# Performance work log

Measured on AMD Instinct MI355X. Metric: run time of the kernel, lower is better.

Reference implementation:

```python
import jax, jax.numpy as jnp
import numpy as np

B, S, H = 2, 2048, 2048
NH, NKV, HD = 16, 4, 128
SCALING = HD ** -0.5


def rotate_half(x):
    x1, x2 = jnp.split(x, 2, axis=-1)
    return jnp.concatenate((-x2, x1), axis=-1)


def apply_rope(t, cos, sin):
    # t: [B, nh, S, HD]; cos/sin: [B, S, HD] -> unsqueeze head dim
    c = cos[:, None, :, :]
    s = sin[:, None, :, :]
    return t * c + rotate_half(t) * s


def setup_inputs() -> dict:
    key = jax.random.key(0)
    k1, k2, k3, k4, k5 = jax.random.split(key, 5)
    hidden_states = jax.random.normal(k1, (B, S, H), dtype=jnp.float32)
    # real RoPE tables
    inv_freq = 1.0 / (10000.0 ** (jnp.arange(0, HD, 2, dtype=jnp.float32) / HD))
    pos = jnp.arange(S, dtype=jnp.float32)
    freqs = jnp.einsum('s,d->sd', pos, inv_freq)              # [S, HD/2]
    emb = jnp.concatenate((freqs, freqs), axis=-1)            # [S, HD]
    cos = jnp.broadcast_to(jnp.cos(emb)[None], (B, S, HD))
    sin = jnp.broadcast_to(jnp.sin(emb)[None], (B, S, HD))
    # additive causal mask [B, 1, S, S]
    causal = jnp.triu(jnp.full((S, S), -1e9, dtype=jnp.float32), k=1)
    attention_mask = jnp.broadcast_to(causal[None, None], (B, 1, S, S))
    sc = 0.02
    wq = jax.random.normal(k2, (NH * HD, H), dtype=jnp.float32) * sc
    wk = jax.random.normal(k3, (NKV * HD, H), dtype=jnp.float32) * sc
    wv = jax.random.normal(k4, (NKV * HD, H), dtype=jnp.float32) * sc
    wo = jax.random.normal(k5, (H, NH * HD), dtype=jnp.float32) * sc
    return {"hidden_states": hidden_states, "cos": cos, "sin": sin,
            "attention_mask": attention_mask, "wq": wq, "wk": wk, "wv": wv, "wo": wo}


def reference(hidden_states, cos, sin, attention_mask, wq, wk, wv, wo):
    x = hidden_states
    # fused-style QKV projections (nn.Linear: x @ W.T), split heads -> [B, nh, S, HD]
    q = (x @ wq.T).reshape(B, S, NH, HD).transpose(0, 2, 1, 3)
    k = (x @ wk.T).reshape(B, S, NKV, HD).transpose(0, 2, 1, 3)
    v = (x @ wv.T).reshape(B, S, NKV, HD).transpose(0, 2, 1, 3)
    q = apply_rope(q, cos, sin)
    k = apply_rope(k, cos, sin)
    # GQA: repeat KV heads (repeat_kv)
    n_rep = NH // NKV
    k = jnp.repeat(k, n_rep, axis=1)
    v = jnp.repeat(v, n_rep, axis=1)
    scores = jnp.einsum('bhqd,bhkd->bhqk', q, k) * SCALING + attention_mask
    attn = jax.nn.softmax(scores.astype(jnp.float32), axis=-1).astype(q.dtype)
    out = jnp.einsum('bhqk,bhkd->bhqd', attn, v)
    out = out.transpose(0, 2, 1, 3).reshape(B, S, NH * HD)
    out = out @ wo.T
    return (out, attn)
```

## Files before the change

### kernel.cpp

```cpp
#include <hip/hip_runtime.h>
#include <cstdint>
#include <cstddef>

typedef __bf16 bf16;
typedef __attribute__((ext_vector_type(8))) __bf16 bf16x8;
typedef __attribute__((ext_vector_type(4))) __bf16 bf16x4;
typedef __attribute__((ext_vector_type(4))) float f32x4;

constexpr int B_ = 2, S_ = 2048, H_ = 2048, NH_ = 16, NKV_ = 4, HD_ = 128;
constexpr float SCALE_ = 0.08838834764831845f;

#define GLDS16(g, l)                                                        \
  __builtin_amdgcn_global_load_lds(                                         \
      (const __attribute__((address_space(1))) void*)(g),                   \
      (__attribute__((address_space(3))) void*)(l), 16, 0, 0)

__global__ void cvt_kernel(const float* __restrict__ src, bf16* __restrict__ dst, int n4) {
  int stride = gridDim.x * blockDim.x;
  for (int i = blockIdx.x * blockDim.x + threadIdx.x; i < n4; i += stride) {
    float4 v = reinterpret_cast<const float4*>(src)[i];
    bf16x4 o;
    o[0] = (bf16)v.x; o[1] = (bf16)v.y; o[2] = (bf16)v.z; o[3] = (bf16)v.w;
    reinterpret_cast<bf16x4*>(dst)[i] = o;
  }
}

template <int EPI>
__global__ __launch_bounds__(256) void gemm_bt(const bf16* __restrict__ A,
                                               const bf16* __restrict__ Bm, int K,
                                               bf16* __restrict__ qb, bf16* __restrict__ kb,
                                               bf16* __restrict__ vtb, float* __restrict__ Cout) {
  __shared__ __align__(16) bf16 As[128 * 64];
  __shared__ __align__(16) bf16 Bs[128 * 64];
  const int tid = threadIdx.x;
  const int lane = tid & 63;
  const int wid = tid >> 6;
  const int m0 = blockIdx.x * 128;
  const int n0 = blockIdx.y * 128;
  const int wm = (wid >> 1) * 64, wn = (wid & 1) * 64;
  const int r = lane & 15, g = lane >> 4;
  f32x4 acc[4][4] = {};

  for (int kt = 0; kt < K; kt += 64) {
    __syncthreads();
#pragma unroll
    for (int i = 0; i < 4; ++i) {
      int cb = wid * 256 + i * 64;
      int c = cb + lane;
      int row = c >> 3, cs = (c & 7) ^ (row & 7);
      const bf16* ga = A + (size_t)(m0 + row) * K + kt + cs * 8;
      GLDS16(ga, As + cb * 8);
      const bf16* gb = Bm + (size_t)(n0 + row) * K + kt + cs * 8;
      GLDS16(gb, Bs + cb * 8);
    }
    asm volatile("s_waitcnt vmcnt(0)" ::: "memory");
    __syncthreads();
#pragma unroll
    for (int ks = 0; ks < 2; ++ks) {
      bf16x8 af[4], bfr[4];
#pragma unroll
      for (int fm = 0; fm < 4; ++fm)
        af[fm] = *(const bf16x8*)(As + (wm + fm * 16 + r) * 64 + (((ks * 4 + g) ^ (r & 7)) << 3));
#pragma unroll
      for (int fn = 0; fn < 4; ++fn)
        bfr[fn] = *(const bf16x8*)(Bs + (wn + fn * 16 + r) * 64 + (((ks * 4 + g) ^ (r & 7)) << 3));
#pragma unroll
      for (int fm = 0; fm < 4; ++fm)
#pragma unroll
        for (int fn = 0; fn < 4; ++fn)
          acc[fm][fn] = __builtin_amdgcn_mfma_f32_16x16x32_bf16(af[fm], bfr[fn], acc[fm][fn], 0, 0, 0);
    }
  }

#pragma unroll
  for (int fm = 0; fm < 4; ++fm)
#pragma unroll
    for (int fn = 0; fn < 4; ++fn)
#pragma unroll
      for (int rr = 0; rr < 4; ++rr) {
        int mm = m0 + wm + fm * 16 + g * 4 + rr;
        int nn = n0 + wn + fn * 16 + r;
        float v = acc[fm][fn][rr];
        if (EPI == 1) {
          Cout[(size_t)mm * 2048 + nn] = v;
        } else {
          int b = mm >> 11, s = mm & (S_ - 1);
          int d = nn & 127;
          if (nn < 2048) {
            int h = nn >> 7;
            qb[(((size_t)b * NH_ + h) * S_ + s) * HD_ + d] = (bf16)v;
          } else if (nn < 2560) {
            int h = (nn - 2048) >> 7;
            kb[(((size_t)b * NKV_ + h) * S_ + s) * HD_ + d] = (bf16)v;
          } else {
            int h = (nn - 2560) >> 7;
            vtb[(((size_t)b * NKV_ + h) * HD_ + d) * S_ + s] = (bf16)v;
          }
        }
      }
}

__global__ void rope_kernel(bf16* __restrict__ qb, bf16* __restrict__ kb,
                            const float* __restrict__ cosp, const float* __restrict__ sinp) {
  const int NQ = B_ * NH_ * S_;
  const int NK = B_ * NKV_ * S_;
  int tot = (NQ + NK) * 64;
  for (int t = blockIdx.x * blockDim.x + threadIdx.x; t < tot; t += gridDim.x * blockDim.x) {
    int d = t & 63;
    int rid = t >> 6;
    bf16* base;
    int b, s;
    if (rid < NQ) {
      base = qb + (size_t)rid * HD_;
      s = rid & (S_ - 1);
      b = rid >> 15;
    } else {
      int r2 = rid - NQ;
      base = kb + (size_t)r2 * HD_;
      s = r2 & (S_ - 1);
      b = r2 >> 13;
    }
    float c = cosp[((size_t)b * S_ + s) * HD_ + d];
    float sn = sinp[((size_t)b * S_ + s) * HD_ + d];
    float x1 = (float)base[d], x2 = (float)base[d + 64];
    base[d] = (bf16)(x1 * c - x2 * sn);
    base[d + 64] = (bf16)(x2 * c + x1 * sn);
  }
}

__global__ __launch_bounds__(256) void attn_kernel(const bf16* __restrict__ qb,
                                                   const bf16* __restrict__ kb,
                                                   const bf16* __restrict__ vtb,
                                                   bf16* __restrict__ aob,
                                                   float* __restrict__ attn_out) {
  __shared__ __align__(16) bf16 Qs[64 * 128];
  __shared__ __align__(16) bf16 Ks[64 * 128];
  __shared__ __align__(16) bf16 Vs[128 * 64];
  __shared__ __align__(16) bf16 Ps[64 * 64];
  const int bid = (blockIdx.x & 7) * 128 + (blockIdx.x >> 3);
  const int qt = 31 - (bid & 31);
  const int h = (bid >> 5) & 15;
  const int b = bid >> 9;
  const int kh = h >> 2;
  const int q0 = qt * 64;
  const int tid = threadIdx.x, lane = tid & 63, wid = tid >> 6;
  const int r = lane & 15, g = lane >> 4;

  const bf16* qsrc = qb + (((size_t)b * NH_ + h) * S_ + q0) * HD_;
  const bf16* kbase = kb + ((size_t)b * NKV_ + kh) * S_ * HD_;
  const bf16* vbase = vtb + ((size_t)b * NKV_ + kh) * (size_t)HD_ * S_;

#pragma unroll
  for (int i = 0; i < 4; ++i) {
    int cb = wid * 256 + i * 64, c = cb + lane;
    int row = c >> 4, cs = (c & 15) ^ (row & 7);
    GLDS16(qsrc + row * 128 + cs * 8, Qs + cb * 8);
  }

  float mrow[4], lrow[4];
#pragma unroll
  for (int i = 0; i < 4; ++i) { mrow[i] = -3e38f; lrow[i] = 0.f; }

  for (int kt = 0; kt <= qt; ++kt) {
    const int k0 = kt * 64;
    __syncthreads();
#pragma unroll
    for (int i = 0; i < 4; ++i) {
      int cb = wid * 256 + i * 64, c = cb + lane;
      int row = c >> 4, cs = (c & 15) ^ (row & 7);
      GLDS16(kbase + (size_t)k0 * HD_ + row * 128 + cs * 8, Ks + cb * 8);
    }
    asm volatile("s_waitcnt vmcnt(0)" ::: "memory");
    __syncthreads();
    f32x4 sacc[4] = {};
#pragma unroll
    for (int ks = 0; ks < 4; ++ks) {
      bf16x8 a = *(const bf16x8*)(Qs + (wid * 16 + r) * 128 + (((ks * 4 + g) ^ (r & 7)) << 3));
#pragma unroll
      for (int fn = 0; fn < 4; ++fn) {
        bf16x8 bb = *(const bf16x8*)(Ks + (fn * 16 + r) * 128 + (((ks * 4 + g) ^ (r & 7)) << 3));
        sacc[fn] = __builtin_amdgcn_mfma_f32_16x16x32_bf16(a, bb, sacc[fn], 0, 0, 0);
      }
    }
    float sv[4][4], tmax[4];
#pragma unroll
    for (int rr = 0; rr < 4; ++rr) tmax[rr] = -3e38f;
#pragma unroll
    for (int fn = 0; fn < 4; ++fn)
#pragma unroll
      for (int rr = 0; rr < 4; ++rr) {
        float s = sacc[fn][rr] * SCALE_;
        if (kt == qt && (fn * 16 + r) > (wid * 16 + g * 4 + rr)) s = -3e38f;
        sv[fn][rr] = s;
        tmax[rr] = fmaxf(tmax[rr], s);
      }
#pragma unroll
    for (int m = 1; m <= 8; m <<= 1)
#pragma unroll
      for (int rr = 0; rr < 4; ++rr) tmax[rr] = fmaxf(tmax[rr], __shfl_xor(tmax[rr], m));
#pragma unroll
    for (int rr = 0; rr < 4; ++rr) {
      float mn = fmaxf(mrow[rr], tmax[rr]);
      float sum = 0.f;
#pragma unroll
      for (int fn = 0; fn < 4; ++fn) sum += __expf(sv[fn][rr] - mn);
#pragma unroll
      for (int m = 1; m <= 8; m <<= 1) sum += __shfl_xor(sum, m);
      lrow[rr] = lrow[rr] * __expf(mrow[rr] - mn) + sum;
      mrow[rr] = mn;
    }
  }

  float rl[4];
#pragma unroll
  for (int rr = 0; rr < 4; ++rr) rl[rr] = 1.0f / lrow[rr];

  f32x4 oacc[8] = {};
  const size_t arow0 = ((size_t)(b * NH_ + h) * S_ + q0) * S_;
  const int trow = tid >> 2;
  const int tcb = (tid & 3) * 16;
  for (int kt = 0; kt <= qt; ++kt) {
    const int k0 = kt * 64;
    __syncthreads();
#pragma unroll
    for (int i = 0; i < 4; ++i) {
      int cb = wid * 256 + i * 64, c = cb + lane;
      int krow = c >> 4, kcs = (c & 15) ^ (krow & 7);
      GLDS16(kbase + (size_t)k0 * HD_ + krow * 128 + kcs * 8, Ks + cb * 8);
      int vrow = c >> 3, vcs = (c & 7) ^ (vrow & 7);
      GLDS16(vbase + (size_t)vrow * S_ + k0 + vcs * 8, Vs + cb * 8);
    }
    asm volatile("s_waitcnt vmcnt(0)" ::: "memory");
    __syncthreads();
    f32x4 sacc[4] = {};
#pragma unroll
    for (int ks = 0; ks < 4; ++ks) {
      bf16x8 a = *(const bf16x8*)(Qs + (wid * 16 + r) * 128 + (((ks * 4 + g) ^ (r & 7)) << 3));
#pragma unroll
      for (int fn = 0; fn < 4; ++fn) {
        bf16x8 bb = *(const bf16x8*)(Ks + (fn * 16 + r) * 128 + (((ks * 4 + g) ^ (r & 7)) << 3));
        sacc[fn] = __builtin_amdgcn_mfma_f32_16x16x32_bf16(a, bb, sacc[fn], 0, 0, 0);
      }
    }
#pragma unroll
    for (int fn = 0; fn < 4; ++fn)
#pragma unroll
      for (int rr = 0; rr < 4; ++rr) {
        float s = sacc[fn][rr] * SCALE_;
        if (kt == qt && (fn * 16 + r) > (wid * 16 + g * 4 + rr)) s = -3e38f;
        float p = __expf(s - mrow[rr]) * rl[rr];
        int qrow = wid * 16 + g * 4 + rr;
        int col = fn * 16 + r;
        Ps[qrow * 64 + ((((col >> 3) ^ (qrow & 7)) << 3) | (col & 7))] = (bf16)p;
      }
    __syncthreads();
    {
      float* dst = attn_out + arow0 + (size_t)trow * S_ + k0 + tcb;
      int ch0 = tcb >> 3;
      bf16x8 p0 = *(const bf16x8*)(Ps + trow * 64 + ((ch0 ^ (trow & 7)) << 3));
      bf16x8 p1 = *(const bf16x8*)(Ps + trow * 64 + (((ch0 + 1) ^ (trow & 7)) << 3));
      float4 o0 = {(float)p0[0], (float)p0[1], (float)p0[2], (float)p0[3]};
      float4 o1 = {(float)p0[4], (float)p0[5], (float)p0[6], (float)p0[7]};
      float4 o2 = {(float)p1[0], (float)p1[1], (float)p1[2], (float)p1[3]};
      float4 o3 = {(float)p1[4], (float)p1[5], (float)p1[6], (float)p1[7]};
      *(float4*)(dst) = o0;
      *(float4*)(dst + 4) = o1;
      *(float4*)(dst + 8) = o2;
      *(float4*)(dst + 12) = o3;
    }
#pragma unroll
    for (int ks = 0; ks < 2; ++ks) {
      bf16x8 pa = *(const bf16x8*)(Ps + (wid * 16 + r) * 64 + (((ks * 4 + g) ^ (r & 7)) << 3));
#pragma unroll
      for (int fn = 0; fn < 8; ++fn) {
        bf16x8 vv = *(const bf16x8*)(Vs + (fn * 16 + r) * 64 + (((ks * 4 + g) ^ (r & 7)) << 3));
        oacc[fn] = __builtin_amdgcn_mfma_f32_16x16x32_bf16(pa, vv, oacc[fn], 0, 0, 0);
      }
    }
  }

  for (int kt = qt + 1; kt < 32; ++kt) {
#pragma unroll
    for (int i = 0; i < 4; ++i) {
      int c = i * 256 + tid;
      int row = c >> 4, col = c & 15;
      float4 z = {0.f, 0.f, 0.f, 0.f};
      *(float4*)(attn_out + arow0 + (size_t)row * S_ + kt * 64 + col * 4) = z;
    }
  }

#pragma unroll
  for (int fn = 0; fn < 8; ++fn)
#pragma unroll
    for (int rr = 0; rr < 4; ++rr) {
      int q = q0 + wid * 16 + g * 4 + rr;
      aob[((size_t)b * S_ + q) * 2048 + h * HD_ + fn * 16 + r] = (bf16)oacc[fn][rr];
    }
}

extern "C" void kernel_launch(void* const* d_in, const int* in_sizes, int n_in,
                              void* d_out, int out_size, void* d_ws, size_t ws_size,
                              hipStream_t stream) {
  const float* hidden = (const float*)d_in[0];
  const float* cosp = (const float*)d_in[1];
  const float* sinp = (const float*)d_in[2];
  const float* wq = (const float*)d_in[4];
  const float* wk = (const float*)d_in[5];
  const float* wv = (const float*)d_in[6];
  const float* wo = (const float*)d_in[7];
  float* out = (float*)d_out;
  float* attn = out + (size_t)B_ * S_ * H_;

  char* ws = (char*)d_ws;
  bf16* xb  = (bf16*)(ws);
  bf16* w3b = (bf16*)(ws + (16ull << 20));
  bf16* wob = (bf16*)(ws + (28ull << 20));
  bf16* qb  = (bf16*)(ws + (36ull << 20));
  bf16* kb  = (bf16*)(ws + (52ull << 20));
  bf16* vtb = (bf16*)(ws + (56ull << 20));
  bf16* aob = (bf16*)(ws + (60ull << 20));

  cvt_kernel<<<2048, 256, 0, stream>>>(hidden, xb, (B_ * S_ * H_) / 4);
  cvt_kernel<<<1024, 256, 0, stream>>>(wq, w3b, (2048 * 2048) / 4);
  cvt_kernel<<<512, 256, 0, stream>>>(wk, w3b + 2048 * 2048, (512 * 2048) / 4);
  cvt_kernel<<<512, 256, 0, stream>>>(wv, w3b + 2560 * 2048, (512 * 2048) / 4);
  cvt_kernel<<<1024, 256, 0, stream>>>(wo, wob, (2048 * 2048) / 4);

  gemm_bt<0><<<dim3(32, 24), 256, 0, stream>>>(xb, w3b, 2048, qb, kb, vtb, nullptr);
  rope_kernel<<<2048, 256, 0, stream>>>(qb, kb, cosp, sinp);
  attn_kernel<<<1024, 256, 0, stream>>>(qb, kb, vtb, aob, attn);
  gemm_bt<1><<<dim3(32, 16), 256, 0, stream>>>(aob, wob, 2048, nullptr, nullptr, nullptr, out);
}
```

Before: 401.6 us.

## Double-buffer GEMM and attention tiles, pair causal q-tiles, fuse conversion kernels

Merges the five fp32-to-bf16 conversion launches into one kernel. Double-buffers the GEMM LDS tiles so the next K-slice is fetched while the current one is multiplied, and adds a grouped block swizzle for L2 reuse. The attention kernel now keeps Q in registers, double-buffers K/V tiles, raises wave priority around MFMA sections, and has each block handle a short and a long causal q-tile pair (p and 31-p) to balance work across 512 blocks. It trades higher LDS use and more complex wait/barrier logic for overlap of loads with compute.

```diff
diff --git a/kernel.cpp b/kernel.cpp
--- a/kernel.cpp
+++ b/kernel.cpp
@@ -15,61 +15,83 @@
       (const __attribute__((address_space(1))) void*)(g),                   \
       (__attribute__((address_space(3))) void*)(l), 16, 0, 0)
 
-__global__ void cvt_kernel(const float* __restrict__ src, bf16* __restrict__ dst, int n4) {
-  int stride = gridDim.x * blockDim.x;
-  for (int i = blockIdx.x * blockDim.x + threadIdx.x; i < n4; i += stride) {
-    float4 v = reinterpret_cast<const float4*>(src)[i];
+#define VMCNT0 asm volatile("s_waitcnt vmcnt(0)" ::: "memory")
+#define VMCNT4 asm volatile("s_waitcnt vmcnt(4)" ::: "memory")
+#define LGKM0 asm volatile("s_waitcnt lgkmcnt(0)" ::: "memory")
+#define BAR __builtin_amdgcn_s_barrier()
+
+__global__ void cvt_all(const float* __restrict__ hs, const float* __restrict__ wq,
+                        const float* __restrict__ wk, const float* __restrict__ wv,
+                        const float* __restrict__ wo, bf16* __restrict__ xb,
+                        bf16* __restrict__ w3b, bf16* __restrict__ wob) {
+  const int stride = gridDim.x * blockDim.x;
+  for (int i = blockIdx.x * blockDim.x + threadIdx.x; i < 4718592; i += stride) {
+    const float4* s; bf16x4* d; int j;
+    if (i < 2097152)      { s = (const float4*)hs; d = (bf16x4*)xb;            j = i; }
+    else if (i < 3145728) { s = (const float4*)wq; d = (bf16x4*)w3b;           j = i - 2097152; }
+    else if (i < 3407872) { s = (const float4*)wk; d = (bf16x4*)w3b + 1048576; j = i - 3145728; }
+    else if (i < 3670016) { s = (const float4*)wv; d = (bf16x4*)w3b + 1310720; j = i - 3407872; }
+    else                  { s = (const float4*)wo; d = (bf16x4*)wob;           j = i - 3670016; }
+    float4 v = s[j];
     bf16x4 o;
     o[0] = (bf16)v.x; o[1] = (bf16)v.y; o[2] = (bf16)v.z; o[3] = (bf16)v.w;
-    reinterpret_cast<bf16x4*>(dst)[i] = o;
+    d[j] = o;
   }
 }
 
 template <int EPI>
-__global__ __launch_bounds__(256) void gemm_bt(const bf16* __restrict__ A,
-                                               const bf16* __restrict__ Bm, int K,
-                                               bf16* __restrict__ qb, bf16* __restrict__ kb,
-                                               bf16* __restrict__ vtb, float* __restrict__ Cout) {
-  __shared__ __align__(16) bf16 As[128 * 64];
-  __shared__ __align__(16) bf16 Bs[128 * 64];
+__global__ __launch_bounds__(256, 2) void gemm_bt(const bf16* __restrict__ A,
+                                                  const bf16* __restrict__ Bm, int K,
+                                                  bf16* __restrict__ qb, bf16* __restrict__ kb,
+                                                  bf16* __restrict__ vtb, float* __restrict__ Cout) {
+  __shared__ __align__(16) bf16 As[2][128 * 64];
+  __shared__ __align__(16) bf16 Bs[2][128 * 64];
   const int tid = threadIdx.x;
   const int lane = tid & 63;
   const int wid = tid >> 6;
-  const int m0 = blockIdx.x * 128;
-  const int n0 = blockIdx.y * 128;
+  const int fid = blockIdx.y * 32 + blockIdx.x;
+  const int nwg = gridDim.y * 32;
+  const int swz = (fid & 7) * (nwg >> 3) + (fid >> 3);
+  const int m0 = (swz & 31) * 128;
+  const int n0 = (swz >> 5) * 128;
   const int wm = (wid >> 1) * 64, wn = (wid & 1) * 64;
   const int r = lane & 15, g = lane >> 4;
   f32x4 acc[4][4] = {};
 
-  for (int kt = 0; kt < K; kt += 64) {
-    __syncthreads();
+  auto STAGE = [&](int kt, int cc) {
 #pragma unroll
     for (int i = 0; i < 4; ++i) {
       int cb = wid * 256 + i * 64;
-      int c = cb + lane;
-      int row = c >> 3, cs = (c & 7) ^ (row & 7);
-      const bf16* ga = A + (size_t)(m0 + row) * K + kt + cs * 8;
-      GLDS16(ga, As + cb * 8);
-      const bf16* gb = Bm + (size_t)(n0 + row) * K + kt + cs * 8;
-      GLDS16(gb, Bs + cb * 8);
-    }
-    asm volatile("s_waitcnt vmcnt(0)" ::: "memory");
-    __syncthreads();
+      int c64 = cb + lane;
+      int row = c64 >> 3, cs = (c64 & 7) ^ (row & 7);
+      GLDS16(A + (size_t)(m0 + row) * K + kt + cs * 8, &As[cc][cb * 8]);
+      GLDS16(Bm + (size_t)(n0 + row) * K + kt + cs * 8, &Bs[cc][cb * 8]);
+    }
+  };
+
+  STAGE(0, 0);
+  VMCNT0; BAR;
+  int c = 0;
+#pragma unroll 1
+  for (int kt = 0; kt < K; kt += 64) {
+    if (kt + 64 < K) STAGE(kt + 64, c ^ 1);
 #pragma unroll
     for (int ks = 0; ks < 2; ++ks) {
       bf16x8 af[4], bfr[4];
 #pragma unroll
       for (int fm = 0; fm < 4; ++fm)
-        af[fm] = *(const bf16x8*)(As + (wm + fm * 16 + r) * 64 + (((ks * 4 + g) ^ (r & 7)) << 3));
+        af[fm] = *(const bf16x8*)(&As[c][(wm + fm * 16 + r) * 64 + (((ks * 4 + g) ^ (r & 7)) << 3)]);
 #pragma unroll
       for (int fn = 0; fn < 4; ++fn)
-        bfr[fn] = *(const bf16x8*)(Bs + (wn + fn * 16 + r) * 64 + (((ks * 4 + g) ^ (r & 7)) << 3));
+        bfr[fn] = *(const bf16x8*)(&Bs[c][(wn + fn * 16 + r) * 64 + (((ks * 4 + g) ^ (r & 7)) << 3)]);
 #pragma unroll
       for (int fm = 0; fm < 4; ++fm)
 #pragma unroll
         for (int fn = 0; fn < 4; ++fn)
           acc[fm][fn] = __builtin_amdgcn_mfma_f32_16x16x32_bf16(af[fm], bfr[fn], acc[fm][fn], 0, 0, 0);
     }
+    VMCNT0; BAR;
+    c ^= 1;
   }
 
 #pragma unroll
@@ -87,14 +109,14 @@
           int b = mm >> 11, s = mm & (S_ - 1);
           int d = nn & 127;
           if (nn < 2048) {
-            int h = nn >> 7;
-            qb[(((size_t)b * NH_ + h) * S_ + s) * HD_ + d] = (bf16)v;
+            int hh = nn >> 7;
+            qb[(((size_t)b * NH_ + hh) * S_ + s) * HD_ + d] = (bf16)v;
           } else if (nn < 2560) {
-            int h = (nn - 2048) >> 7;
-            kb[(((size_t)b * NKV_ + h) * S_ + s) * HD_ + d] = (bf16)v;
+            int hh = (nn - 2048) >> 7;
+            kb[(((size_t)b * NKV_ + hh) * S_ + s) * HD_ + d] = (bf16)v;
           } else {
-            int h = (nn - 2560) >> 7;
-            vtb[(((size_t)b * NKV_ + h) * HD_ + d) * S_ + s] = (bf16)v;
+            int hh = (nn - 2560) >> 7;
+            vtb[(((size_t)b * NKV_ + hh) * HD_ + d) * S_ + s] = (bf16)v;
           }
         }
       }
@@ -128,174 +150,216 @@
   }
 }
 
-__global__ __launch_bounds__(256) void attn_kernel(const bf16* __restrict__ qb,
-                                                   const bf16* __restrict__ kb,
-                                                   const bf16* __restrict__ vtb,
-                                                   bf16* __restrict__ aob,
-                                                   float* __restrict__ attn_out) {
-  __shared__ __align__(16) bf16 Qs[64 * 128];
-  __shared__ __align__(16) bf16 Ks[64 * 128];
-  __shared__ __align__(16) bf16 Vs[128 * 64];
+__global__ __launch_bounds__(256, 2) void attn_kernel(const bf16* __restrict__ qb,
+                                                      const bf16* __restrict__ kb,
+                                                      const bf16* __restrict__ vtb,
+                                                      bf16* __restrict__ aob,
+                                                      float* __restrict__ attn_out) {
+  __shared__ __align__(16) bf16 Ks[2][64 * 128];
+  __shared__ __align__(16) bf16 Vs[2][128 * 64];
   __shared__ __align__(16) bf16 Ps[64 * 64];
-  const int bid = (blockIdx.x & 7) * 128 + (blockIdx.x >> 3);
-  const int qt = 31 - (bid & 31);
-  const int h = (bid >> 5) & 15;
-  const int b = bid >> 9;
+  const int bid = (blockIdx.x & 7) * 64 + (blockIdx.x >> 3);
+  const int p = bid & 15;
+  const int h = (bid >> 4) & 15;
+  const int b = bid >> 8;
   const int kh = h >> 2;
-  const int q0 = qt * 64;
   const int tid = threadIdx.x, lane = tid & 63, wid = tid >> 6;
   const int r = lane & 15, g = lane >> 4;
 
-  const bf16* qsrc = qb + (((size_t)b * NH_ + h) * S_ + q0) * HD_;
   const bf16* kbase = kb + ((size_t)b * NKV_ + kh) * S_ * HD_;
   const bf16* vbase = vtb + ((size_t)b * NKV_ + kh) * (size_t)HD_ * S_;
 
-#pragma unroll
-  for (int i = 0; i < 4; ++i) {
-    int cb = wid * 256 + i * 64, c = cb + lane;
-    int row = c >> 4, cs = (c & 15) ^ (row & 7);
-    GLDS16(qsrc + row * 128 + cs * 8, Qs + cb * 8);
-  }
-
-  float mrow[4], lrow[4];
-#pragma unroll
-  for (int i = 0; i < 4; ++i) { mrow[i] = -3e38f; lrow[i] = 0.f; }
-
-  for (int kt = 0; kt <= qt; ++kt) {
-    const int k0 = kt * 64;
-    __syncthreads();
+  auto stageK = [&](int kt, int cc) {
 #pragma unroll
     for (int i = 0; i < 4; ++i) {
-      int cb = wid * 256 + i * 64, c = cb + lane;
-      int row = c >> 4, cs = (c & 15) ^ (row & 7);
-      GLDS16(kbase + (size_t)k0 * HD_ + row * 128 + cs * 8, Ks + cb * 8);
-    }
-    asm volatile("s_waitcnt vmcnt(0)" ::: "memory");
-    __syncthreads();
-    f32x4 sacc[4] = {};
-#pragma unroll
-    for (int ks = 0; ks < 4; ++ks) {
-      bf16x8 a = *(const bf16x8*)(Qs + (wid * 16 + r) * 128 + (((ks * 4 + g) ^ (r & 7)) << 3));
-#pragma unroll
-      for (int fn = 0; fn < 4; ++fn) {
-        bf16x8 bb = *(const bf16x8*)(Ks + (fn * 16 + r) * 128 + (((ks * 4 + g) ^ (r & 7)) << 3));
-        sacc[fn] = __builtin_amdgcn_mfma_f32_16x16x32_bf16(a, bb, sacc[fn], 0, 0, 0);
-      }
-    }
-    float sv[4][4], tmax[4];
-#pragma unroll
-    for (int rr = 0; rr < 4; ++rr) tmax[rr] = -3e38f;
-#pragma unroll
-    for (int fn = 0; fn < 4; ++fn)
+      int base = i * 256 + wid * 64;
+      int idx = base + lane;
+      int row = idx >> 4, ch = (idx & 15) ^ (row & 7);
+      GLDS16(kbase + (size_t)(kt * 64 + row) * HD_ + ch * 8, &Ks[cc][base * 8]);
+    }
+  };
+  auto stageV = [&](int kt, int cc) {
+#pragma unroll
+    for (int i = 0; i < 4; ++i) {
+      int base = i * 256 + wid * 64;
+      int idx = base + lane;
+      int row = idx >> 3, ch = (idx & 7) ^ (row & 7);
+      GLDS16(vbase + (size_t)row * S_ + kt * 64 + ch * 8, &Vs[cc][base * 8]);
+    }
+  };
+
+#pragma unroll 1
+  for (int sbi = 0; sbi < 2; ++sbi) {
+    const int qt = sbi ? 31 - p : p;
+    const int q0 = qt * 64;
+    const int nt = qt + 1;
+    const bf16* qsrc = qb + (((size_t)b * NH_ + h) * S_ + q0) * HD_;
+
+    bf16x8 qreg[4];
+#pragma unroll
+    for (int ks = 0; ks < 4; ++ks)
+      qreg[ks] = *(const bf16x8*)(qsrc + (wid * 16 + r) * HD_ + ks * 32 + g * 8);
+
+    float mrow[4], lrow[4];
+#pragma unroll
+    for (int rr = 0; rr < 4; ++rr) { mrow[rr] = -3e38f; lrow[rr] = 0.f; }
+
+    stageK(0, 0);
+    VMCNT0; BAR;
+    int c = 0;
+#pragma unroll 1
+    for (int kt = 0; kt < nt; ++kt) {
+      if (kt + 1 < nt) stageK(kt + 1, c ^ 1);
+      f32x4 sacc[4] = {};
+      __builtin_amdgcn_s_setprio(1);
+#pragma unroll
+      for (int ks = 0; ks < 4; ++ks)
+#pragma unroll
+        for (int fn = 0; fn < 4; ++fn) {
+          bf16x8 bb = *(const bf16x8*)(&Ks[c][(fn * 16 + r) * 128 + (((ks * 4 + g) ^ (r & 7)) << 3)]);
+          sacc[fn] = __builtin_amdgcn_mfma_f32_16x16x32_bf16(qreg[ks], bb, sacc[fn], 0, 0, 0);
+        }
+      __builtin_amdgcn_s_setprio(0);
+      const int k0 = kt * 64;
+      if (kt == nt - 1) {
+#pragma unroll
+        for (int fn = 0; fn < 4; ++fn)
+#pragma unroll
+          for (int rr = 0; rr < 4; ++rr) {
+            bool msk = (k0 + fn * 16 + r) > (q0 + wid * 16 + g * 4 + rr);
+            sacc[fn][rr] = msk ? -3e38f : sacc[fn][rr] * SCALE_;
+          }
+      } else {
+#pragma unroll
+        for (int fn = 0; fn < 4; ++fn)
+#pragma unroll
+          for (int rr = 0; rr < 4; ++rr) sacc[fn][rr] *= SCALE_;
+      }
+      float tmax[4] = {-3e38f, -3e38f, -3e38f, -3e38f};
+#pragma unroll
+      for (int fn = 0; fn < 4; ++fn)
+#pragma unroll
+        for (int rr = 0; rr < 4; ++rr) tmax[rr] = fmaxf(tmax[rr], sacc[fn][rr]);
+#pragma unroll
+      for (int m = 1; m <= 8; m <<= 1)
+#pragma unroll
+        for (int rr = 0; rr < 4; ++rr) tmax[rr] = fmaxf(tmax[rr], __shfl_xor(tmax[rr], m));
 #pragma unroll
       for (int rr = 0; rr < 4; ++rr) {
-        float s = sacc[fn][rr] * SCALE_;
-        if (kt == qt && (fn * 16 + r) > (wid * 16 + g * 4 + rr)) s = -3e38f;
-        sv[fn][rr] = s;
-        tmax[rr] = fmaxf(tmax[rr], s);
-      }
-#pragma unroll
-    for (int m = 1; m <= 8; m <<= 1)
-#pragma unroll
-      for (int rr = 0; rr < 4; ++rr) tmax[rr] = fmaxf(tmax[rr], __shfl_xor(tmax[rr], m));
-#pragma unroll
-    for (int rr = 0; rr < 4; ++rr) {
-      float mn = fmaxf(mrow[rr], tmax[rr]);
-      float sum = 0.f;
-#pragma unroll
-      for (int fn = 0; fn < 4; ++fn) sum += __expf(sv[fn][rr] - mn);
-#pragma unroll
-      for (int m = 1; m <= 8; m <<= 1) sum += __shfl_xor(sum, m);
-      lrow[rr] = lrow[rr] * __expf(mrow[rr] - mn) + sum;
-      mrow[rr] = mn;
-    }
-  }
-
-  float rl[4];
-#pragma unroll
-  for (int rr = 0; rr < 4; ++rr) rl[rr] = 1.0f / lrow[rr];
-
-  f32x4 oacc[8] = {};
-  const size_t arow0 = ((size_t)(b * NH_ + h) * S_ + q0) * S_;
-  const int trow = tid >> 2;
-  const int tcb = (tid & 3) * 16;
-  for (int kt = 0; kt <= qt; ++kt) {
-    const int k0 = kt * 64;
-    __syncthreads();
-#pragma unroll
-    for (int i = 0; i < 4; ++i) {
-      int cb = wid * 256 + i * 64, c = cb + lane;
-      int krow = c >> 4, kcs = (c & 15) ^ (krow & 7);
-      GLDS16(kbase + (size_t)k0 * HD_ + krow * 128 + kcs * 8, Ks + cb * 8);
-      int vrow = c >> 3, vcs = (c & 7) ^ (vrow & 7);
-      GLDS16(vbase + (size_t)vrow * S_ + k0 + vcs * 8, Vs + cb * 8);
-    }
-    asm volatile("s_waitcnt vmcnt(0)" ::: "memory");
-    __syncthreads();
-    f32x4 sacc[4] = {};
-#pragma unroll
-    for (int ks = 0; ks < 4; ++ks) {
-      bf16x8 a = *(const bf16x8*)(Qs + (wid * 16 + r) * 128 + (((ks * 4 + g) ^ (r & 7)) << 3));
-#pragma unroll
-      for (int fn = 0; fn < 4; ++fn) {
-        bf16x8 bb = *(const bf16x8*)(Ks + (fn * 16 + r) * 128 + (((ks * 4 + g) ^ (r & 7)) << 3));
-        sacc[fn] = __builtin_amdgcn_mfma_f32_16x16x32_bf16(a, bb, sacc[fn], 0, 0, 0);
-      }
-    }
-#pragma unroll
-    for (int fn = 0; fn < 4; ++fn)
+        float mn = fmaxf(mrow[rr], tmax[rr]);
+        float sum = 0.f;
+#pragma unroll
+        for (int fn = 0; fn < 4; ++fn) sum += __expf(sacc[fn][rr] - mn);
+#pragma unroll
+        for (int m = 1; m <= 8; m <<= 1) sum += __shfl_xor(sum, m);
+        lrow[rr] = lrow[rr] * __expf(mrow[rr] - mn) + sum;
+        mrow[rr] = mn;
+      }
+      VMCNT0; BAR;
+      c ^= 1;
+    }
+
+    float rl[4];
+#pragma unroll
+    for (int rr = 0; rr < 4; ++rr) rl[rr] = 1.0f / lrow[rr];
+
+    f32x4 oacc[8] = {};
+    const size_t arow0 = ((size_t)(b * NH_ + h) * S_ + q0) * S_;
+    stageK(0, 0);
+    stageV(0, 0);
+    VMCNT0; BAR;
+    c = 0;
+#pragma unroll 1
+    for (int kt = 0; kt < nt; ++kt) {
+      if (kt + 1 < nt) { stageK(kt + 1, c ^ 1); stageV(kt + 1, c ^ 1); }
+      const int k0 = kt * 64;
+      f32x4 sacc[4] = {};
+      __builtin_amdgcn_s_setprio(1);
+#pragma unroll
+      for (int ks = 0; ks < 4; ++ks)
+#pragma unroll
+        for (int fn = 0; fn < 4; ++fn) {
+          bf16x8 bb = *(const bf16x8*)(&Ks[c][(fn * 16 + r) * 128 + (((ks * 4 + g) ^ (r & 7)) << 3)]);
+          sacc[fn] = __builtin_amdgcn_mfma_f32_16x16x32_bf16(qreg[ks], bb, sacc[fn], 0, 0, 0);
+        }
+      __builtin_amdgcn_s_setprio(0);
+      if (kt == nt - 1) {
+#pragma unroll
+        for (int fn = 0; fn < 4; ++fn)
+#pragma unroll
+          for (int rr = 0; rr < 4; ++rr) {
+            bool msk = (k0 + fn * 16 + r) > (q0 + wid * 16 + g * 4 + rr);
+            sacc[fn][rr] = msk ? -3e38f : sacc[fn][rr] * SCALE_;
+          }
+      } else {
+#pragma unroll
+        for (int fn = 0; fn < 4; ++fn)
+#pragma unroll
+          for (int rr = 0; rr < 4; ++rr) sacc[fn][rr] *= SCALE_;
+      }
+#pragma unroll
+      for (int fn = 0; fn < 4; ++fn)
+#pragma unroll
+        for (int rr = 0; rr < 4; ++rr) {
+          float pv = __expf(sacc[fn][rr] - mrow[rr]) * rl[rr];
+          int qrow = wid * 16 + g * 4 + rr, col = fn * 16 + r;
+          Ps[qrow * 64 + ((((col >> 3) ^ (qrow & 7)) << 3) | (col & 7))] = (bf16)pv;
+        }
+      LGKM0; BAR;
+      {
+        const int trow = tid >> 2, tcb = (tid & 3) * 16;
+        float* dst = attn_out + arow0 + (size_t)trow * S_ + k0 + tcb;
+        int ch0 = (tid & 3) * 2;
+        bf16x8 p0 = *(const bf16x8*)(&Ps[trow * 64 + ((ch0 ^ (trow & 7)) << 3)]);
+        bf16x8 p1 = *(const bf16x8*)(&Ps[trow * 64 + (((ch0 + 1) ^ (trow & 7)) << 3)]);
+        float4 o0 = {(float)p0[0], (float)p0[1], (float)p0[2], (float)p0[3]};
+        float4 o1 = {(float)p0[4], (float)p0[5], (float)p0[6], (float)p0[7]};
+        float4 o2 = {(float)p1[0], (float)p1[1], (float)p1[2], (float)p1[3]};
+        float4 o3 = {(float)p1[4], (float)p1[5], (float)p1[6], (float)p1[7]};
+        *(float4*)(dst) = o0;
+        *(float4*)(dst + 4) = o1;
+        *(float4*)(dst + 8) = o2;
+        *(float4*)(dst + 12) = o3;
+      }
+      __builtin_amdgcn_s_setprio(1);
+#pragma unroll
+      for (int ks = 0; ks < 2; ++ks) {
+        bf16x8 pa = *(const bf16x8*)(&Ps[(wid * 16 + r) * 64 + (((ks * 4 + g) ^ (r & 7)) << 3)]);
+#pragma unroll
+        for (int fn = 0; fn < 8; ++fn) {
+          bf16x8 vv = *(const bf16x8*)(&Vs[c][(fn * 16 + r) * 64 + (((ks * 4 + g) ^ (r & 7)) << 3)]);
+          oacc[fn] = __builtin_amdgcn_mfma_f32_16x16x32_bf16(pa, vv, oacc[fn], 0, 0, 0);
+        }
+      }
+      __builtin_amdgcn_s_setprio(0);
+      VMCNT4; BAR;
+      c ^= 1;
+    }
+
+#pragma unroll
+    for (int fn = 0; fn < 8; ++fn)
 #pragma unroll
       for (int rr = 0; rr < 4; ++rr) {
-        float s = sacc[fn][rr] * SCALE_;
-        if (kt == qt && (fn * 16 + r) > (wid * 16 + g * 4 + rr)) s = -3e38f;
-        float p = __expf(s - mrow[rr]) * rl[rr];
-        int qrow = wid * 16 + g * 4 + rr;
-        int col = fn * 16 + r;
-        Ps[qrow * 64 + ((((col >> 3) ^ (qrow & 7)) << 3) | (col & 7))] = (bf16)p;
-      }
-    __syncthreads();
-    {
-      float* dst = attn_out + arow0 + (size_t)trow * S_ + k0 + tcb;
-      int ch0 = tcb >> 3;
-      bf16x8 p0 = *(const bf16x8*)(Ps + trow * 64 + ((ch0 ^ (trow & 7)) << 3));
-      bf16x8 p1 = *(const bf16x8*)(Ps + trow * 64 + (((ch0 + 1) ^ (trow & 7)) << 3));
-      float4 o0 = {(float)p0[0], (float)p0[1], (float)p0[2], (float)p0[3]};
-      float4 o1 = {(float)p0[4], (float)p0[5], (float)p0[6], (float)p0[7]};
-      float4 o2 = {(float)p1[0], (float)p1[1], (float)p1[2], (float)p1[3]};
-      float4 o3 = {(float)p1[4], (float)p1[5], (float)p1[6], (float)p1[7]};
-      *(float4*)(dst) = o0;
-      *(float4*)(dst + 4) = o1;
-      *(float4*)(dst + 8) = o2;
-      *(float4*)(dst + 12) = o3;
-    }
-#pragma unroll
-    for (int ks = 0; ks < 2; ++ks) {
-      bf16x8 pa = *(const bf16x8*)(Ps + (wid * 16 + r) * 64 + (((ks * 4 + g) ^ (r & 7)) << 3));
-#pragma unroll
-      for (int fn = 0; fn < 8; ++fn) {
-        bf16x8 vv = *(const bf16x8*)(Vs + (fn * 16 + r) * 64 + (((ks * 4 + g) ^ (r & 7)) << 3));
-        oacc[fn] = __builtin_amdgcn_mfma_f32_16x16x32_bf16(pa, vv, oacc[fn], 0, 0, 0);
-      }
-    }
-  }
-
-  for (int kt = qt + 1; kt < 32; ++kt) {
-#pragma unroll
-    for (int i = 0; i < 4; ++i) {
-      int c = i * 256 + tid;
-      int row = c >> 4, col = c & 15;
-      float4 z = {0.f, 0.f, 0.f, 0.f};
-      *(float4*)(attn_out + arow0 + (size_t)row * S_ + kt * 64 + col * 4) = z;
-    }
-  }
-
-#pragma unroll
-  for (int fn = 0; fn < 8; ++fn)
-#pragma unroll
-    for (int rr = 0; rr < 4; ++rr) {
-      int q = q0 + wid * 16 + g * 4 + rr;
-      aob[((size_t)b * S_ + q) * 2048 + h * HD_ + fn * 16 + r] = (bf16)oacc[fn][rr];
-    }
+        int q = q0 + wid * 16 + g * 4 + rr;
+        aob[((size_t)b * S_ + q) * 2048 + h * HD_ + fn * 16 + r] = (bf16)oacc[fn][rr];
+      }
+  }
+
+#pragma unroll 1
+  for (int sbi = 0; sbi < 2; ++sbi) {
+    const int qt = sbi ? 31 - p : p;
+    const size_t arow0 = ((size_t)(b * NH_ + h) * S_ + qt * 64) * S_;
+#pragma unroll 1
+    for (int kt2 = qt + 1; kt2 < 32; ++kt2) {
+#pragma unroll
+      for (int i = 0; i < 4; ++i) {
+        int cidx = i * 256 + tid;
+        int row = cidx >> 4, colq = cidx & 15;
+        float4 z = {0.f, 0.f, 0.f, 0.f};
+        *(float4*)(attn_out + arow0 + (size_t)row * S_ + kt2 * 64 + colq * 4) = z;
+      }
+    }
+  }
 }
 
 extern "C" void kernel_launch(void* const* d_in, const int* in_sizes, int n_in,
@@ -320,14 +384,9 @@
   bf16* vtb = (bf16*)(ws + (56ull << 20));
   bf16* aob = (bf16*)(ws + (60ull << 20));
 
-  cvt_kernel<<<2048, 256, 0, stream>>>(hidden, xb, (B_ * S_ * H_) / 4);
-  cvt_kernel<<<1024, 256, 0, stream>>>(wq, w3b, (2048 * 2048) / 4);
-  cvt_kernel<<<512, 256, 0, stream>>>(wk, w3b + 2048 * 2048, (512 * 2048) / 4);
-  cvt_kernel<<<512, 256, 0, stream>>>(wv, w3b + 2560 * 2048, (512 * 2048) / 4);
-  cvt_kernel<<<1024, 256, 0, stream>>>(wo, wob, (2048 * 2048) / 4);
-
+  cvt_all<<<2048, 256, 0, stream>>>(hidden, wq, wk, wv, wo, xb, w3b, wob);
   gemm_bt<0><<<dim3(32, 24), 256, 0, stream>>>(xb, w3b, 2048, qb, kb, vtb, nullptr);
   rope_kernel<<<2048, 256, 0, stream>>>(qb, kb, cosp, sinp);
-  attn_kernel<<<1024, 256, 0, stream>>>(qb, kb, vtb, aob, attn);
+  attn_kernel<<<512, 256, 0, stream>>>(qb, kb, vtb, aob, attn);
   gemm_bt<1><<<dim3(32, 16), 256, 0, stream>>>(aob, wob, 2048, nullptr, nullptr, nullptr, out);
 }
```

New measurement: 380.0 us. -5.4%, faster.
